# Optimization experiments

Hardware: AMD Instinct MI355X
Metric: run time of the kernel (lower is better)

The kernel has to match this reference:

```python
import jax, jax.numpy as jnp
import numpy as np

K = 7            # attention window
HEADS = 8
C_ATT = 32       # in_channels of AttBlock
DKH = C_ATT // HEADS  # 4
C_FC = 512       # resnet18 fc channels
NUM_CLASS = 20


def conv2d(x, w, b, stride=1, padding=0):
    out = jax.lax.conv_general_dilated(
        x, w, (stride, stride), [(padding, padding), (padding, padding)],
        dimension_numbers=("NCHW", "OIHW", "NCHW"))
    return out + b[None, :, None, None]


def unfold2(t, k, H, W):
    # torch t.unfold(2,k,1).unfold(3,k,1): [B,C,Hp,Wp] -> [B,C,H,W,k,k]
    t = jnp.stack([t[:, :, i:i + H, :] for i in range(k)], axis=-1)      # [B,C,H,Wp,k]
    t = jnp.stack([t[:, :, :, j:j + W, :] for j in range(k)], axis=-1)   # [B,C,H,W,k,k]
    return t


def bilinear_resize(x, oh, ow):
    # torch F.interpolate(mode='bilinear', align_corners=False)
    B, C, H, W = x.shape
    ys = jnp.clip((jnp.arange(oh, dtype=x.dtype) + 0.5) * (H / oh) - 0.5, 0, H - 1)
    xs = jnp.clip((jnp.arange(ow, dtype=x.dtype) + 0.5) * (W / ow) - 0.5, 0, W - 1)
    y0 = jnp.floor(ys).astype(jnp.int32); y1 = jnp.minimum(y0 + 1, H - 1)
    x0 = jnp.floor(xs).astype(jnp.int32); x1 = jnp.minimum(x0 + 1, W - 1)
    wy = (ys - y0)[None, None, :, None]
    wx = (xs - x0)[None, None, None, :]
    g = lambda yi, xi: x[:, :, yi][:, :, :, xi]
    top = g(y0, x0) * (1 - wx) + g(y0, x1) * wx
    bot = g(y1, x0) * (1 - wx) + g(y1, x1) * wx
    return top * (1 - wy) + bot * wy


def att_block(x, conv1_w, conv1_b, k_w, k_b, q_w, q_b, v_w, v_b, rel_h, rel_w):
    B, _, H, W = x.shape
    x1 = conv2d(x, conv1_w, conv1_b, padding=1)                    # [B,32,H,W]
    p = (K - 1) // 2
    xp = jnp.pad(x1, ((0, 0), (0, 0), (p, K - 1 - p), (p, K - 1 - p)))
    k = conv2d(xp, k_w, k_b)                                       # [B,32,H+6,W+6]
    q = conv2d(x1, q_w, q_b)                                       # [B,32,H,W]
    v = conv2d(xp, v_w, v_b)
    k = unfold2(k, K, H, W).reshape(B, HEADS, H, W, DKH, -1)       # raw row-major reshape (as torch)
    v = unfold2(v, K, H, W).reshape(B, HEADS, H, W, DKH, -1)
    q = q.reshape(B, HEADS, H, W, DKH, 1)
    qk = jnp.matmul(jnp.swapaxes(q, 4, 5), k).reshape(B, HEADS, H, W, K, K)
    # einsum 'bhxydz,cij->bhxyij' fully contracts d,z,c -> outer product of sums
    qsum = q.sum(axis=(4, 5))                                      # [B,heads,H,W]
    rel = rel_h.sum(0) + rel_w.sum(0)                              # [K,1]+[1,K] -> [K,K]
    qk = qk + qsum[..., None, None] * rel
    w = jax.nn.softmax(qk.reshape(B, HEADS, H, W, 1, K * K), axis=-1)
    attn = jnp.matmul(w, jnp.swapaxes(v, 4, 5))                    # [B,heads,H,W,1,dvh]
    return attn.reshape(B, -1, H, W)                               # [B,32,H,W]


def setup_inputs() -> dict:
    key = jax.random.key(0)
    ks = jax.random.split(key, 16)
    s = 0.05
    inp = {
        "x": jax.random.normal(ks[0], (1, 6, 256, 256), jnp.float32),
        "diff_input": 1,
        "backbone_w": jax.random.normal(ks[1], (C_FC, 6, 3, 3), jnp.float32) * s,
        "backbone_b": jax.random.normal(ks[2], (C_FC,), jnp.float32) * s,
        "conv1_w": jax.random.normal(ks[3], (C_ATT, 6, 3, 3), jnp.float32) * s,
        "conv1_b": jax.random.normal(ks[4], (C_ATT,), jnp.float32) * s,
        "k_w": jax.random.normal(ks[5], (C_ATT, C_ATT, 1, 1), jnp.float32) * s,
        "k_b": jax.random.normal(ks[6], (C_ATT,), jnp.float32) * s,
        "q_w": jax.random.normal(ks[7], (C_ATT, C_ATT, 1, 1), jnp.float32) * s,
        "q_b": jax.random.normal(ks[8], (C_ATT,), jnp.float32) * s,
        "v_w": jax.random.normal(ks[9], (C_ATT, C_ATT, 1, 1), jnp.float32) * s,
        "v_b": jax.random.normal(ks[10], (C_ATT,), jnp.float32) * s,
        "rel_h": jax.random.normal(ks[11], (C_ATT // 2, K, 1), jnp.float32),
        "rel_w": jax.random.normal(ks[12], (C_ATT // 2, 1, K), jnp.float32),
        "expand_w": jax.random.normal(ks[13], (C_FC, C_ATT, 3, 3), jnp.float32) * s,
        "expand_b": jax.random.normal(ks[14], (C_FC,), jnp.float32) * s,
        "fc_w": jax.random.normal(ks[15], (NUM_CLASS, C_FC), jnp.float32) * s,
        "fc_b": jnp.zeros((NUM_CLASS,), jnp.float32),
    }
    return inp


def reference(x, diff_input, backbone_w, backbone_b, conv1_w, conv1_b,
              k_w, k_b, q_w, q_b, v_w, v_b, rel_h, rel_w,
              expand_w, expand_b, fc_w, fc_b):
    # multi_task_model stub: stride-8 conv trunk -> [B,512,H/8,W/8]
    res_out = conv2d(x, backbone_w, backbone_b, stride=8, padding=1)
    # diff_input is not None -> attention branch always taken
    att_res = att_block(x, conv1_w, conv1_b, k_w, k_b, q_w, q_b, v_w, v_b, rel_h, rel_w)
    att_scale = bilinear_resize(att_res, res_out.shape[2], res_out.shape[3])
    att_enhance = res_out + conv2d(att_scale, expand_w, expand_b, padding=1)
    pooled = att_enhance.mean(axis=(2, 3))          # AdaptiveAvgPool2d((1,1))
    fc_x = pooled @ fc_w.T + fc_b                   # [B,num_class]
    return fc_x
```

## Files before the change

### kernel.cpp

```cpp
#include <hip/hip_runtime.h>
#include <math.h>


#define OFF_STATA ((size_t)0)
#define OFF_SX    ((size_t)3072)
#define OFF_P     ((size_t)3136)
#define OFF_MG    ((size_t)3648)
#define OFF_MB    ((size_t)9024)
#define OFF_RW    ((size_t)9280)

#define SM_KT   0
#define SM_VT   2176
#define SM_QS   4352
#define SM_ML   4864
#define SM_BIAS 5032
#define SM_RW   5040
#define SM_RED  5056
#define SM_TOT  5120

__global__ __launch_bounds__(256) void k_prep(
    const float* __restrict__ x,
    const float* __restrict__ c1w, const float* __restrict__ c1b,
    const float* __restrict__ kw, const float* __restrict__ kb,
    const float* __restrict__ qw, const float* __restrict__ qb,
    const float* __restrict__ vw, const float* __restrict__ vb,
    const float* __restrict__ relh, const float* __restrict__ relw,
    float* __restrict__ MG, float* __restrict__ MB,
    float* __restrict__ RW, float* __restrict__ Sx) {
  int b = blockIdx.x, t = threadIdx.x;
  if (b < 32) {
    int c = b;
    if (t < 168) {
      int ci = t / 28, s = t - ci * 28;
      float a = 0.f;
      if (s < 27) {
        int kind = s / 9, t9 = s - kind * 9;
        const float* w3 = (kind == 0 ? kw : (kind == 1 ? vw : qw)) + c * 32;
        #pragma unroll
        for (int m = 0; m < 32; ++m)
          a = fmaf(w3[m], c1w[(m * 6 + ci) * 9 + t9], a);
      }
      MG[c * 168 + t] = a;
    } else if (t < 176) {
      int s = t - 168;
      float a = 0.f;
      if (s < 3) {
        const float* w3 = (s == 0 ? kw : (s == 1 ? vw : qw)) + c * 32;
        a = (s == 0 ? kb : (s == 1 ? vb : qb))[c];
        #pragma unroll
        for (int m = 0; m < 32; ++m) a = fmaf(w3[m], c1b[m], a);
      } else if (s == 3) a = kb[c];
      else if (s == 4) a = vb[c];
      MB[c * 8 + s] = a;
    }
    return;
  }
  if (b < 86) {
    int e = b - 32;
    int ci = e / 9, rem = e - ci * 9, ky = rem / 3, kx = rem - ky * 3;
    const float* xc = x + (size_t)ci * 65536;
    float acc = 0.f;
    for (int p = t; p < 1024; p += 256) {
      int oy = p >> 5, ox = p & 31;
      int ry = 8 * oy - 1 + ky, cx = 8 * ox - 1 + kx;
      if (ry >= 0 && ry <= 255 && cx >= 0 && cx <= 255)
        acc += xc[ry * 256 + cx];
    }
    #pragma unroll
    for (int off = 32; off >= 1; off >>= 1) acc += __shfl_down(acc, off);
    __shared__ float part[4];
    if ((t & 63) == 0) part[t >> 6] = acc;
    __syncthreads();
    if (t == 0) Sx[e] = part[0] + part[1] + part[2] + part[3];
    return;
  }
  if (t < 16) {
    float s = 0.f;
    if (t < 7) {
      for (int cc = 0; cc < 16; ++cc) s += relh[cc * 7 + t];
    } else if (t >= 8 && t < 15) {
      int j = t - 8;
      for (int cc = 0; cc < 16; ++cc) s += relw[cc * 7 + j];
    }
    RW[t] = s;
  }
}

__global__ __launch_bounds__(256) void k_fused(
    const float* __restrict__ x,
    const float* __restrict__ MG, const float* __restrict__ MB,
    const float* __restrict__ RW, float* __restrict__ statA) {
  __shared__ float smem[SM_TOT];
  int tid = threadIdx.x;
  int c  = blockIdx.x >> 5;
  int oy = blockIdx.x & 31;

  float* KT  = smem + SM_KT;
  float* VT  = smem + SM_VT;
  float* QS  = smem + SM_QS;
  float* Ml  = smem + SM_ML;
  float* bsl = smem + SM_BIAS;
  float* rhs = smem + SM_RW;
  float* rws = smem + SM_RW + 8;
  float* red = smem + SM_RED;

  if (tid < 168)      Ml[tid] = MG[c * 168 + tid];
  else if (tid < 176) bsl[tid - 168] = MB[c * 8 + (tid - 168)];
  else if (tid < 192) smem[SM_RW + (tid - 176)] = RW[tid - 176];
  __syncthreads();

  int cg = tid & 63, rg = tid >> 6;
  int roq = (rg == 1) ? 1 : ((rg == 2) ? 0 : -1);
  float kacc[2][4], vacc[2][4], qacc[4];
  {
    float mk = bsl[0], mv = bsl[1], mq = bsl[2];
    #pragma unroll
    for (int ro = 0; ro < 2; ++ro)
      #pragma unroll
      for (int cc = 0; cc < 4; ++cc) { kacc[ro][cc] = mk; vacc[ro][cc] = mv; }
    #pragma unroll
    for (int cc = 0; cc < 4; ++cc) qacc[cc] = mq;
  }
  float mA = (cg > 0) ? 1.0f : 0.0f;
  float mC = (cg < 63) ? 1.0f : 0.0f;
  int xr0 = 8 * oy + 2 * rg - 1;

  #pragma unroll 1
  for (int ci = 0; ci < 6; ++ci) {
    const float* xch = x + (size_t)ci * 65536;
    float wch[28];
    {
      const float4* Mc = (const float4*)&Ml[ci * 28];
      *(float4*)&wch[0]  = Mc[0]; *(float4*)&wch[4]  = Mc[1];
      *(float4*)&wch[8]  = Mc[2]; *(float4*)&wch[12] = Mc[3];
      *(float4*)&wch[16] = Mc[4]; *(float4*)&wch[20] = Mc[5];
      *(float4*)&wch[24] = Mc[6];
    }
    #pragma unroll
    for (int s4 = 0; s4 < 4; ++s4) {
      int xr = xr0 + s4;
      float mrow = (xr >= 0 && xr <= 255) ? 1.0f : 0.0f;
      int xrc = min(max(xr, 0), 255);
      float4 Bv = *(const float4*)&xch[xrc * 256 + 4 * cg];
      float left  = __shfl_up(Bv.w, 1);
      float right = __shfl_down(Bv.x, 1);
      float win[6];
      win[0] = left  * (mA * mrow);
      win[1] = Bv.x * mrow;
      win[2] = Bv.y * mrow;
      win[3] = Bv.z * mrow;
      win[4] = Bv.w * mrow;
      win[5] = right * (mC * mrow);
      if (s4 < 3) {
        const float* wk = &wch[3 * s4];
        const float* wv = &wch[9 + 3 * s4];
        #pragma unroll
        for (int cc = 0; cc < 4; ++cc) {
          float a = kacc[0][cc], b2 = vacc[0][cc];
          #pragma unroll
          for (int dxw = 0; dxw < 3; ++dxw) {
            float xv = win[cc + dxw];
            a  = fmaf(wk[dxw], xv, a);
            b2 = fmaf(wv[dxw], xv, b2);
          }
          kacc[0][cc] = a; vacc[0][cc] = b2;
        }
        if (roq == 0) {
          const float* wq = &wch[18 + 3 * s4];
          #pragma unroll
          for (int cc = 0; cc < 4; ++cc) {
            float qa = qacc[cc];
            #pragma unroll
            for (int dxw = 0; dxw < 3; ++dxw)
              qa = fmaf(wq[dxw], win[cc + dxw], qa);
            qacc[cc] = qa;
          }
        }
      }
      if (s4 >= 1) {
        const float* wk = &wch[3 * (s4 - 1)];
        const float* wv = &wch[9 + 3 * (s4 - 1)];
        #pragma unroll
        for (int cc = 0; cc < 4; ++cc) {
          float a = kacc[1][cc], b2 = vacc[1][cc];
          #pragma unroll
          for (int dxw = 0; dxw < 3; ++dxw) {
            float xv = win[cc + dxw];
            a  = fmaf(wk[dxw], xv, a);
            b2 = fmaf(wv[dxw], xv, b2);
          }
          kacc[1][cc] = a; vacc[1][cc] = b2;
        }
        if (roq == 1) {
          const float* wq = &wch[18 + 3 * (s4 - 1)];
          #pragma unroll
          for (int cc = 0; cc < 4; ++cc) {
            float qa = qacc[cc];
            #pragma unroll
            for (int dxw = 0; dxw < 3; ++dxw)
              qa = fmaf(wq[dxw], win[cc + dxw], qa);
            qacc[cc] = qa;
          }
        }
      }
    }
  }

  #pragma unroll
  for (int ro = 0; ro < 2; ++ro) {
    int r = 2 * rg + ro;
    *(float4*)&KT[r * 272 + 4 * cg + 4] =
        make_float4(kacc[ro][0], kacc[ro][1], kacc[ro][2], kacc[ro][3]);
    *(float4*)&VT[r * 272 + 4 * cg + 4] =
        make_float4(vacc[ro][0], vacc[ro][1], vacc[ro][2], vacc[ro][3]);
  }
  if (roq >= 0)
    *(float4*)&QS[(rg == 2 ? 256 : 0) + 4 * cg] =
        make_float4(qacc[0], qacc[1], qacc[2], qacc[3]);
  if (tid < 96) {
    int t2 = tid;
    int kv = t2 >= 48; if (kv) t2 -= 48;
    int lr = t2 & 7, pi = t2 >> 3;
    int slot = (pi < 3) ? (pi + 1) : (pi + 257);
    (kv ? VT : KT)[lr * 272 + slot] = bsl[3 + kv];
  }
  __syncthreads();

  {
    int half = tid & 1;
    int pix  = tid >> 1;
    int dx   = pix & 1;
    int ox   = (pix >> 1) & 31;
    int dy   = (pix >> 6) & 1;
    int wb   = 8 * ox + 4 * dx;
    int dv   = dx ? 0 : 3;
    int i0   = half * 3;

    float4 qv4 = *(const float4*)&QS[dy * 256 + wb];
    float qv0 = qv4.x, qv1 = qv4.y, qv2 = qv4.z, qv3 = qv4.w;
    float qsum = qv0 + qv1 + qv2 + qv3;

    float sum = 0.f, o = 0.f;
    #pragma unroll
    for (int ii = 0; ii < 4; ++ii) {
      int i = i0 + ii;
      float act = ((half == 0) || (ii > 0)) ? 1.0f : 0.0f;
      const float* kr = &KT[(dy + i) * 272 + wb];
      const float* vr = &VT[(dy + i) * 272 + wb];
      float B[12], BV[12];
      *(float4*)&B[0]  = *(const float4*)&kr[0];
      *(float4*)&B[4]  = *(const float4*)&kr[4];
      *(float4*)&B[8]  = *(const float4*)&kr[8];
      *(float4*)&BV[0] = *(const float4*)&vr[0];
      *(float4*)&BV[4] = *(const float4*)&vr[4];
      *(float4*)&BV[8] = *(const float4*)&vr[8];
      float rh = rhs[i];
      #pragma unroll
      for (int j = 0; j < 7; ++j) {
        float d0 = fmaf(qv0, B[j + 1],
                   fmaf(qv1, B[j + 2],
                   fmaf(qv2, B[j + 3], qv3 * B[j + 4])));
        float s = fmaf(qsum, rh + rws[j], d0);
        float e = act * __expf(s);
        sum += e;
        o = fmaf(e, BV[dv + j + 1], o);
      }
    }
    sum += __shfl_xor(sum, 1);
    o   += __shfl_xor(o, 1);

    float quarter = 0.25f * o / sum;
    float psum = quarter + __shfl_xor(quarter, 2);
    if ((tid & 3) == 0) red[dy * 32 + ox] = psum;
  }
  __syncthreads();

  if (tid < 32) {
    float scv = red[tid] + red[32 + tid];
    float e0  = __shfl(scv, 0, 32);
    float e31 = __shfl(scv, 31, 32);
    float rs = scv;
    #pragma unroll
    for (int off = 16; off >= 1; off >>= 1) rs += __shfl_down(rs, off, 32);
    if (tid == 0) {
      float* pa = statA + (c * 32 + oy) * 3;
      pa[0] = rs; pa[1] = e0; pa[2] = e31;
    }
  }
}

__global__ __launch_bounds__(64) void k_pool(
    const float* __restrict__ statA, const float* __restrict__ Sx,
    const float* __restrict__ bw, const float* __restrict__ bb,
    const float* __restrict__ ew, const float* __restrict__ eb,
    float* __restrict__ pooled) {
  __shared__ float Sl[342];
  int oc = blockIdx.x, lane = threadIdx.x;
  if (lane < 32) {
    int ch = lane;
    const float* pa = statA + ch * 96;
    float T = 0.f, C0 = 0.f, C31 = 0.f;
    #pragma unroll
    for (int i = 0; i < 32; ++i) {
      T += pa[3 * i]; C0 += pa[3 * i + 1]; C31 += pa[3 * i + 2];
    }
    float r0 = pa[0],  e00 = pa[1],    e0_31 = pa[2];
    float r31 = pa[93], e31_0 = pa[94], e31_31 = pa[95];
    #pragma unroll
    for (int ky = 0; ky < 3; ++ky) {
      float exR = (ky == 0) ? r31 : (ky == 2 ? r0 : 0.f);
      #pragma unroll
      for (int kx = 0; kx < 3; ++kx) {
        float exC = (kx == 0) ? C31 : (kx == 2 ? C0 : 0.f);
        float corner = 0.f;
        if (ky != 1 && kx != 1) {
          if (ky == 0) corner = (kx == 0) ? e31_31 : e31_0;
          else         corner = (kx == 0) ? e0_31  : e00;
        }
        Sl[ch * 9 + ky * 3 + kx] = T - exR - exC + corner;
      }
    }
  }
  if (lane < 54) Sl[288 + lane] = Sx[lane];
  __syncthreads();

  float acc = 0.f;
  #pragma unroll
  for (int i0 = 0; i0 < 342; i0 += 64) {
    int i = i0 + lane;
    if (i < 342) {
      float wv = (i < 288) ? ew[oc * 288 + i] : bw[oc * 54 + (i - 288)];
      acc = fmaf(wv, Sl[i], acc);
    }
  }
  #pragma unroll
  for (int off = 32; off >= 1; off >>= 1) acc += __shfl_down(acc, off);
  if (lane == 0)
    pooled[oc] = bb[oc] + eb[oc] + acc * (1.0f / 1024.0f);
}

__global__ __launch_bounds__(64) void k_fc(
    const float* __restrict__ pooled, const float* __restrict__ fcw,
    const float* __restrict__ fcb, float* __restrict__ out) {
  int o = blockIdx.x, lane = threadIdx.x;
  float acc = 0.f;
  #pragma unroll
  for (int i0 = 0; i0 < 512; i0 += 64)
    acc = fmaf(fcw[o * 512 + i0 + lane], pooled[i0 + lane], acc);
  #pragma unroll
  for (int off = 32; off >= 1; off >>= 1) acc += __shfl_down(acc, off);
  if (lane == 0) out[o] = fcb[o] + acc;
}

extern "C" void kernel_launch(void* const* d_in, const int* in_sizes, int n_in,
                              void* d_out, int out_size, void* d_ws, size_t ws_size,
                              hipStream_t stream) {
  const float* x    = (const float*)d_in[0];
  const float* bw   = (const float*)d_in[2];
  const float* bb   = (const float*)d_in[3];
  const float* c1w  = (const float*)d_in[4];
  const float* c1b  = (const float*)d_in[5];
  const float* kw   = (const float*)d_in[6];
  const float* kb   = (const float*)d_in[7];
  const float* qw   = (const float*)d_in[8];
  const float* qb   = (const float*)d_in[9];
  const float* vw   = (const float*)d_in[10];
  const float* vb   = (const float*)d_in[11];
  const float* relh = (const float*)d_in[12];
  const float* relw = (const float*)d_in[13];
  const float* ew   = (const float*)d_in[14];
  const float* eb   = (const float*)d_in[15];
  const float* fcw  = (const float*)d_in[16];
  const float* fcb  = (const float*)d_in[17];

  float* ws    = (float*)d_ws;
  float* statA = ws + OFF_STATA;
  float* Sxb   = ws + OFF_SX;
  float* pool  = ws + OFF_P;
  float* MG    = ws + OFF_MG;
  float* MB    = ws + OFF_MB;
  float* RW    = ws + OFF_RW;
  float* out   = (float*)d_out;

  k_prep <<<87,   256, 0, stream>>>(x, c1w, c1b, kw, kb, qw, qb, vw, vb,
                                    relh, relw, MG, MB, RW, Sxb);
  k_fused<<<1024, 256, 0, stream>>>(x, MG, MB, RW, statA);
  k_pool <<<512,  64,  0, stream>>>(statA, Sxb, bw, bb, ew, eb, pool);
  k_fc   <<<20,   64,  0, stream>>>(pool, fcw, fcb, out);
}
```

Baseline: 33.87 us.

## Fold fc weights into expand/backbone weights in prep, merge pool and fc kernels

The fc layer is linear, so the prep kernel now precomputes G = fc_w·expand_w and Gb = fc_w·backbone_w, plus a combined bias (fc_w·(bb+eb)+fc_b). These weight-only products run in parallel with the other prep blocks. The final stage then becomes a single 20-block kernel that dots the precomputed statistics with G/Gb, replacing the 512-block pool kernel and the separate fc kernel. This saves one launch and the intermediate pooled buffer, at the cost of extra prep work that re-multiplies weight-only products on every call.

```diff
diff --git a/kernel.cpp b/kernel.cpp
--- a/kernel.cpp
+++ b/kernel.cpp
@@ -4,10 +4,12 @@
 
 #define OFF_STATA ((size_t)0)
 #define OFF_SX    ((size_t)3072)
-#define OFF_P     ((size_t)3136)
-#define OFF_MG    ((size_t)3648)
-#define OFF_MB    ((size_t)9024)
-#define OFF_RW    ((size_t)9280)
+#define OFF_MG    ((size_t)3136)
+#define OFF_MB    ((size_t)8512)
+#define OFF_RW    ((size_t)8768)
+#define OFF_G     ((size_t)8800)
+#define OFF_GB    ((size_t)14560)
+#define OFF_FCB2  ((size_t)15640)
 
 #define SM_KT   0
 #define SM_VT   2176
@@ -25,9 +27,16 @@
     const float* __restrict__ qw, const float* __restrict__ qb,
     const float* __restrict__ vw, const float* __restrict__ vb,
     const float* __restrict__ relh, const float* __restrict__ relw,
+    const float* __restrict__ bw, const float* __restrict__ bb,
+    const float* __restrict__ ew, const float* __restrict__ eb,
+    const float* __restrict__ fcw, const float* __restrict__ fcb,
     float* __restrict__ MG, float* __restrict__ MB,
-    float* __restrict__ RW, float* __restrict__ Sx) {
+    float* __restrict__ RW, float* __restrict__ Sx,
+    float* __restrict__ G, float* __restrict__ Gb,
+    float* __restrict__ FCB2) {
   int b = blockIdx.x, t = threadIdx.x;
+  __shared__ float red2[256];
+
   if (b < 32) {
     int c = b;
     if (t < 168) {
@@ -68,21 +77,58 @@
     }
     #pragma unroll
     for (int off = 32; off >= 1; off >>= 1) acc += __shfl_down(acc, off);
-    __shared__ float part[4];
-    if ((t & 63) == 0) part[t >> 6] = acc;
+    if ((t & 63) == 0) red2[t >> 6] = acc;
     __syncthreads();
-    if (t == 0) Sx[e] = part[0] + part[1] + part[2] + part[3];
+    if (t == 0) Sx[e] = red2[0] + red2[1] + red2[2] + red2[3];
     return;
   }
-  if (t < 16) {
-    float s = 0.f;
-    if (t < 7) {
-      for (int cc = 0; cc < 16; ++cc) s += relh[cc * 7 + t];
-    } else if (t >= 8 && t < 15) {
-      int j = t - 8;
-      for (int cc = 0; cc < 16; ++cc) s += relw[cc * 7 + j];
-    }
-    RW[t] = s;
+  if (b == 86) {
+    if (t < 16) {
+      float s = 0.f;
+      if (t < 7) {
+        for (int cc = 0; cc < 16; ++cc) s += relh[cc * 7 + t];
+      } else if (t >= 8 && t < 15) {
+        int j = t - 8;
+        for (int cc = 0; cc < 16; ++cc) s += relw[cc * 7 + j];
+      }
+      RW[t] = s;
+    }
+    return;
+  }
+  if (b < 194) {
+    int gi0 = (b - 87) * 64;
+    int l = t & 63, w = t >> 6;
+    int g = gi0 + l;
+    int o = g / 342;
+    int i = g - o * 342;
+    bool valid = (g < 6840);
+    int oc = valid ? o : 0;
+    float acc = 0.f;
+    const float* fr = fcw + oc * 512;
+    #pragma unroll 8
+    for (int mm = 0; mm < 128; ++mm) {
+      int m = w * 128 + mm;
+      float val = (i < 288) ? ew[m * 288 + i] : bw[m * 54 + (i - 288)];
+      acc = fmaf(fr[m], val, acc);
+    }
+    red2[t] = acc;
+    __syncthreads();
+    if (w == 0 && valid) {
+      float s = red2[l] + red2[64 + l] + red2[128 + l] + red2[192 + l];
+      if (i < 288) G[o * 288 + i] = s;
+      else         Gb[o * 54 + (i - 288)] = s;
+    }
+    return;
+  }
+  {
+    int o = b - 194;
+    float acc = fmaf(fcw[o * 512 + t], bb[t] + eb[t],
+                     fcw[o * 512 + 256 + t] * (bb[256 + t] + eb[256 + t]));
+    #pragma unroll
+    for (int off = 32; off >= 1; off >>= 1) acc += __shfl_down(acc, off);
+    if ((t & 63) == 0) red2[t >> 6] = acc;
+    __syncthreads();
+    if (t == 0) FCB2[o] = fcb[o] + red2[0] + red2[1] + red2[2] + red2[3];
   }
 }
 
@@ -289,13 +335,13 @@
   }
 }
 
-__global__ __launch_bounds__(64) void k_pool(
+__global__ __launch_bounds__(64) void k_out(
     const float* __restrict__ statA, const float* __restrict__ Sx,
-    const float* __restrict__ bw, const float* __restrict__ bb,
-    const float* __restrict__ ew, const float* __restrict__ eb,
-    float* __restrict__ pooled) {
-  __shared__ float Sl[342];
-  int oc = blockIdx.x, lane = threadIdx.x;
+    const float* __restrict__ G, const float* __restrict__ Gb,
+    const float* __restrict__ FCB2, float* __restrict__ out) {
+  __shared__ float Sl[288];
+  __shared__ float SxL[54];
+  int o = blockIdx.x, lane = threadIdx.x;
   if (lane < 32) {
     int ch = lane;
     const float* pa = statA + ch * 96;
@@ -320,36 +366,21 @@
         Sl[ch * 9 + ky * 3 + kx] = T - exR - exC + corner;
       }
     }
-  }
-  if (lane < 54) Sl[288 + lane] = Sx[lane];
+  } else {
+    for (int idx = lane - 32; idx < 54; idx += 32) SxL[idx] = Sx[idx];
+  }
   __syncthreads();
 
   float acc = 0.f;
   #pragma unroll
-  for (int i0 = 0; i0 < 342; i0 += 64) {
+  for (int i0 = 0; i0 < 288; i0 += 64) {
     int i = i0 + lane;
-    if (i < 342) {
-      float wv = (i < 288) ? ew[oc * 288 + i] : bw[oc * 54 + (i - 288)];
-      acc = fmaf(wv, Sl[i], acc);
-    }
-  }
+    if (i < 288) acc = fmaf(G[o * 288 + i], Sl[i], acc);
+  }
+  if (lane < 54) acc = fmaf(Gb[o * 54 + lane], SxL[lane], acc);
   #pragma unroll
   for (int off = 32; off >= 1; off >>= 1) acc += __shfl_down(acc, off);
-  if (lane == 0)
-    pooled[oc] = bb[oc] + eb[oc] + acc * (1.0f / 1024.0f);
-}
-
-__global__ __launch_bounds__(64) void k_fc(
-    const float* __restrict__ pooled, const float* __restrict__ fcw,
-    const float* __restrict__ fcb, float* __restrict__ out) {
-  int o = blockIdx.x, lane = threadIdx.x;
-  float acc = 0.f;
-  #pragma unroll
-  for (int i0 = 0; i0 < 512; i0 += 64)
-    acc = fmaf(fcw[o * 512 + i0 + lane], pooled[i0 + lane], acc);
-  #pragma unroll
-  for (int off = 32; off >= 1; off >>= 1) acc += __shfl_down(acc, off);
-  if (lane == 0) out[o] = fcb[o] + acc;
+  if (lane == 0) out[o] = FCB2[o] + acc * (1.0f / 1024.0f);
 }
 
 extern "C" void kernel_launch(void* const* d_in, const int* in_sizes, int n_in,
@@ -376,15 +407,17 @@
   float* ws    = (float*)d_ws;
   float* statA = ws + OFF_STATA;
   float* Sxb   = ws + OFF_SX;
-  float* pool  = ws + OFF_P;
   float* MG    = ws + OFF_MG;
   float* MB    = ws + OFF_MB;
   float* RW    = ws + OFF_RW;
+  float* Gm    = ws + OFF_G;
+  float* Gbm   = ws + OFF_GB;
+  float* FCB2  = ws + OFF_FCB2;
   float* out   = (float*)d_out;
 
-  k_prep <<<87,   256, 0, stream>>>(x, c1w, c1b, kw, kb, qw, qb, vw, vb,
-                                    relh, relw, MG, MB, RW, Sxb);
+  k_prep <<<214,  256, 0, stream>>>(x, c1w, c1b, kw, kb, qw, qb, vw, vb,
+                                    relh, relw, bw, bb, ew, eb, fcw, fcb,
+                                    MG, MB, RW, Sxb, Gm, Gbm, FCB2);
   k_fused<<<1024, 256, 0, stream>>>(x, MG, MB, RW, statA);
-  k_pool <<<512,  64,  0, stream>>>(statA, Sxb, bw, bb, ew, eb, pool);
-  k_fc   <<<20,   64,  0, stream>>>(pool, fcw, fcb, out);
+  k_out  <<<20,   64,  0, stream>>>(statA, Sxb, Gm, Gbm, FCB2, out);
 }
```

Result: slower. 35.60 us (+5.1%).
